# Performance work log

Measured on AMD Instinct MI355X. Metric: run time of the kernel, lower is better.

Reference implementation:

```python
import jax, jax.numpy as jnp
import numpy as np

BN_EPS = 1e-3
EPS = 1e-8
IGNORE = -1


def _head(x, w1, b1, g, be, w2, b2):
    # Linear -> BatchNorm1d (training: batch stats, biased var) -> ReLU -> Linear
    h = x @ w1 + b1
    mu = h.mean(axis=0)
    var = h.var(axis=0)  # biased, matches torch BN normalization
    h = (h - mu) * jax.lax.rsqrt(var + BN_EPS) * g + be
    h = jax.nn.relu(h)
    return h @ w2 + b2


def _bias_losses(a, b, mask):
    # faithful to compute_loss(bias_gt, bias_pred, mask); l1 and cosine are symmetric
    dist = jnp.sum(jnp.abs(a - b), axis=-1)
    denom = jnp.sum(mask) + EPS
    l1 = jnp.sum(dist * mask) / denom
    an = a / (jnp.linalg.norm(a, axis=-1, keepdims=True) + EPS)
    bn = b / (jnp.linalg.norm(b, axis=-1, keepdims=True) + EPS)
    cos = -jnp.sum(an * bn, axis=-1)
    cl = jnp.sum(cos * mask) / denom
    return l1, cl


def setup_inputs() -> dict:
    key = jax.random.key(0)
    ks = jax.random.split(key, 12)
    N, C, S = 1048576, 64, 20
    inp = {
        'feat': jax.random.normal(ks[0], (N, C), jnp.float32),
        'coord': jax.random.normal(ks[1], (N, 3), jnp.float32) * 2.0,
        'segment': jax.random.randint(ks[2], (N,), -1, S).astype(jnp.int32),
        'instance': jax.random.randint(ks[3], (N,), -1, 200).astype(jnp.int32),
        'instance_centroid': jax.random.normal(ks[4], (N, 3), jnp.float32) * 2.0,
        'w1_xy': jax.random.normal(ks[5], (C, C), jnp.float32) * 0.05,
        'b1_xy': jnp.zeros((C,), jnp.float32),
        'g_xy': jnp.ones((C,), jnp.float32),
        'be_xy': jnp.zeros((C,), jnp.float32),
        'w2_xy': jax.random.normal(ks[6], (C, 2), jnp.float32) * 0.05,
        'b2_xy': jnp.zeros((2,), jnp.float32),
        'w1_z': jax.random.normal(ks[7], (C, C), jnp.float32) * 0.05,
        'b1_z': jnp.zeros((C,), jnp.float32),
        'g_z': jnp.ones((C,), jnp.float32),
        'be_z': jnp.zeros((C,), jnp.float32),
        'w2_z': jax.random.normal(ks[8], (C, 1), jnp.float32) * 0.05,
        'b2_z': jnp.zeros((1,), jnp.float32),
        'w_seg': jax.random.normal(ks[9], (C, S), jnp.float32) * 0.05,
        'b_seg': jnp.zeros((S,), jnp.float32),
    }
    return inp


def reference(feat, coord, segment, instance, instance_centroid,
              w1_xy, b1_xy, g_xy, be_xy, w2_xy, b2_xy,
              w1_z, b1_z, g_z, be_z, w2_z, b2_z,
              w_seg, b_seg):
    bias_pred_xy = _head(feat, w1_xy, b1_xy, g_xy, be_xy, w2_xy, b2_xy)  # [N,2]
    bias_pred_z = _head(feat, w1_z, b1_z, g_z, be_z, w2_z, b2_z)         # [N,1]
    logit_pred = feat @ w_seg + b_seg                                     # [N,S]

    # cross-entropy with ignore_index=-1, unit class weights
    valid = (segment != IGNORE)
    tgt = jnp.where(valid, segment, 0)
    logp = jax.nn.log_softmax(logit_pred, axis=-1)
    nll = -jnp.take_along_axis(logp, tgt[:, None], axis=1)[:, 0]
    vf = valid.astype(logit_pred.dtype)
    seg_loss = jnp.sum(nll * vf) / jnp.sum(vf)

    mask = (instance != IGNORE).astype(feat.dtype)
    bias_gt = instance_centroid - coord
    l1_xy, cos_xy = _bias_losses(bias_gt[:, :2], bias_pred_xy, mask)
    l1_z, cos_z = _bias_losses(bias_gt[:, 2:3], bias_pred_z, mask)

    # faithful to original (bias_xy_l1 counted twice, xy cosine unused in total)
    loss = seg_loss + l1_xy + l1_xy + 0.5 * (l1_z + cos_z)
    return (loss, seg_loss, l1_xy, cos_xy, l1_z, cos_z)
```

## Files before the change

kernel.cpp:

```cpp
#include <hip/hip_runtime.h>
#include <hip/hip_bf16.h>

#define OFF_COLSUM 0
#define OFF_S      64
#define OFF_SHX    4160
#define OFF_SHZ    4224
#define OFF_ACC    4288
#define OFF_W1XS   4304
#define OFF_W1ZS   6352
#define OFF_WSEGS  8400

typedef __attribute__((ext_vector_type(8))) short bf16x8;
typedef __attribute__((ext_vector_type(4))) float f32x4;

__device__ __forceinline__ unsigned short f2bfh(float x) {
    __hip_bfloat16 h = __float2bfloat16(x);
    return *reinterpret_cast<unsigned short*>(&h);
}

union BF8 { bf16x8 v; unsigned short u[8]; };

__device__ __forceinline__ void gload_lds16(const void* g, void* l) {
    __builtin_amdgcn_global_load_lds((const __attribute__((address_space(1))) void*)g,
                                     (__attribute__((address_space(3))) void*)l, 16, 0, 0);
}


__global__ __launch_bounds__(256, 2) void k_stats(const float* __restrict__ feat,
                                                  int N, int ntiles, int tpb,
                                                  float* __restrict__ ws) {
    __shared__ __align__(16) float ftile[2][4096];
    const int t = threadIdx.x;
    const int lane = t & 63, l15 = lane & 15, grp = lane >> 4, wv = t >> 6;

    const f32x4 z4 = {0.f, 0.f, 0.f, 0.f};
    f32x4 acc[4] = {z4, z4, z4, z4};
    float csum = 0.f;

    const int l3 = l15 & 3;
    const int cb_base = l15 >> 2;
    const int g1x8 = (grp & 1) * 8;

    const int ti0 = blockIdx.x * tpb;
    const int tiend = min(ti0 + tpb, ntiles);

    auto stage = [&](int bufi, int ti) {
        const int row0 = ti * 64;
        if (row0 + 64 <= N) {
#pragma unroll
            for (int c = 0; c < 4; c++) {
                const int r = (wv * 4 + c) * 4 + grp;
                const int u = l15 ^ (r & 15);
                gload_lds16(&feat[(size_t)(row0 + r) * 64 + u * 4],
                            &ftile[bufi][(wv * 4 + c) * 256]);
            }
        } else {
#pragma unroll
            for (int u2 = 0; u2 < 4; u2++) {
                const int i = t + u2 * 256;
                const int r = i >> 4, u = (i & 15) ^ (r & 15);
                float4 v = make_float4(0.f, 0.f, 0.f, 0.f);
                if (row0 + r < N) v = *(const float4*)&feat[(size_t)(row0 + r) * 64 + u * 4];
                *(float4*)&ftile[bufi][i * 4] = v;
            }
        }
    };

    if (ti0 < tiend) stage(0, ti0);
    int cur = 0;
    for (int ti = ti0; ti < tiend; ++ti) {
        __syncthreads();
        if (ti + 1 < tiend) stage(cur ^ 1, ti + 1);
        const float* fb = ftile[cur];

        bf16x8 fr[4][2];
#pragma unroll
        for (int s = 0; s < 4; s++) {
            const int g = (wv + s) & 3;
            const int cb = (g * 4 + cb_base) ^ g1x8;
#pragma unroll
            for (int h = 0; h < 2; h++) {
                const int pbase = h * 32 + grp * 8;
                float vs[8];
#pragma unroll
                for (int kk = 0; kk < 8; kk++)
                    vs[kk] = fb[(pbase + kk) * 64 + ((cb ^ kk) << 2) + l3];
                BF8 fv;
#pragma unroll
                for (int kk = 0; kk < 8; kk++) fv.u[kk] = f2bfh(vs[kk]);
                fr[s][h] = fv.v;
                if (s == 0) {
#pragma unroll
                    for (int kk = 0; kk < 8; kk++) csum += vs[kk];
                }
            }
        }
#pragma unroll
        for (int s = 0; s < 4; s++) {
            acc[s] = __builtin_amdgcn_mfma_f32_16x16x32_bf16(fr[0][0], fr[s][0], acc[s], 0, 0, 0);
            acc[s] = __builtin_amdgcn_mfma_f32_16x16x32_bf16(fr[0][1], fr[s][1], acc[s], 0, 0, 0);
        }
        cur ^= 1;
    }

    float* S = ws + OFF_S;
#pragma unroll
    for (int s = 0; s < 4; s++) {
        const int gj = (wv + s) & 3;
#pragma unroll
        for (int r = 0; r < 4; r++)
            atomicAdd(&S[(wv * 16 + grp * 4 + r) * 64 + gj * 16 + l15], acc[s][r]);
    }
    csum += __shfl_xor(csum, 16);
    csum += __shfl_xor(csum, 32);
    if (grp == 0) atomicAdd(&ws[OFF_COLSUM + wv * 16 + l15], csum);
}

__global__ __launch_bounds__(256) void k_prep(
    const float* __restrict__ w1xy, const float* __restrict__ b1xy,
    const float* __restrict__ gxy,  const float* __restrict__ bexy,
    const float* __restrict__ w1z,  const float* __restrict__ b1z,
    const float* __restrict__ gz,   const float* __restrict__ bez,
    const float* __restrict__ wseg, float Nf, float* __restrict__ ws) {
    __shared__ float S[64][64];
    __shared__ float cs[64];
    const int t = threadIdx.x;

    for (int i = t; i < 4096; i += 256) ((float*)S)[i] = ws[OFF_S + i];
    if (t < 64) cs[t] = ws[OFF_COLSUM + t];
    __syncthreads();

    if (t < 128) {
        const int head = t >> 6, j = t & 63;
        const float* w1 = head ? w1z : w1xy;
        float w[64];
#pragma unroll
        for (int k = 0; k < 64; k++) w[k] = w1[k * 64 + j];
        float d = 0.f;
#pragma unroll
        for (int k = 0; k < 64; k++) d = fmaf(cs[k], w[k], d);
        float quad = 0.f;
#pragma unroll
        for (int k = 0; k < 64; k++) {
            float rd = 0.f;
#pragma unroll
            for (int l = 0; l < 64; l++) rd = fmaf(S[k][l], w[l], rd);
            quad = fmaf(w[k], rd, quad);
        }
        const float b1 = head ? b1z[j] : b1xy[j];
        const float mu  = d / Nf + b1;
        const float eh2 = quad / Nf + 2.f * b1 * d / Nf + b1 * b1;
        const float var = eh2 - mu * mu;
        const float g  = head ? gz[j]  : gxy[j];
        const float be = head ? bez[j] : bexy[j];
        const float sc = g * rsqrtf(var + 1e-3f);
        const float sh = be - mu * sc;
        ws[(head ? OFF_SHZ : OFF_SHX) + j] = sh;
        unsigned short* dst = (unsigned short*)(ws + (head ? OFF_W1ZS : OFF_W1XS));
#pragma unroll
        for (int k = 0; k < 64; k++) dst[j * 64 + k] = f2bfh(w[k] * sc);
    } else if (t < 160) {
        const int j = t - 128;
        unsigned short* dst = (unsigned short*)(ws + OFF_WSEGS);
        for (int k = 0; k < 64; k++)
            dst[j * 64 + k] = (j < 20) ? f2bfh(wseg[k * 20 + j]) : (unsigned short)0;
    }
}

__global__ __launch_bounds__(256, 2) void k_loss(
    const float* __restrict__ feat, const float* __restrict__ coord,
    const int* __restrict__ seg, const int* __restrict__ inst,
    const float* __restrict__ cent,
    const unsigned short* __restrict__ w1xs, const unsigned short* __restrict__ w1zs,
    const unsigned short* __restrict__ wsegs,
    const float* __restrict__ shxv, const float* __restrict__ shzv,
    const float* __restrict__ w2xy, const float* __restrict__ b2xy,
    const float* __restrict__ w2z,  const float* __restrict__ b2z,
    const float* __restrict__ bseg,
    int N, int ntiles, int tpb, float* __restrict__ acc) {
    __shared__ __align__(16) float ftile[2][4096];
    __shared__ float red[4][8];

    const int t = threadIdx.x;
    const int lane = t & 63, l15 = lane & 15, grp = lane >> 4, wv = t >> 6;

    bf16x8 ax[4][2], az[4][2], ag[2][2];
#pragma unroll
    for (int nt = 0; nt < 4; nt++)
#pragma unroll
        for (int h = 0; h < 2; h++) {
            ax[nt][h] = *(const bf16x8*)&w1xs[(nt * 16 + l15) * 64 + grp * 8 + h * 32];
            az[nt][h] = *(const bf16x8*)&w1zs[(nt * 16 + l15) * 64 + grp * 8 + h * 32];
        }
#pragma unroll
    for (int nt = 0; nt < 2; nt++)
#pragma unroll
        for (int h = 0; h < 2; h++)
            ag[nt][h] = *(const bf16x8*)&wsegs[(nt * 16 + l15) * 64 + grp * 8 + h * 32];

    float shx_c[4][4], shz_c[4][4], w20[4][4], w21[4][4], w2zc[4][4], bs_c[2][4];
#pragma unroll
    for (int nt = 0; nt < 4; nt++)
#pragma unroll
        for (int r = 0; r < 4; r++) {
            const int c = nt * 16 + grp * 4 + r;
            shx_c[nt][r] = shxv[c]; shz_c[nt][r] = shzv[c];
            w20[nt][r] = w2xy[c * 2]; w21[nt][r] = w2xy[c * 2 + 1];
            w2zc[nt][r] = w2z[c];
        }
#pragma unroll
    for (int nt = 0; nt < 2; nt++)
#pragma unroll
        for (int r = 0; r < 4; r++) {
            const int c = nt * 16 + grp * 4 + r;
            bs_c[nt][r] = (c < 20) ? bseg[c] : -1e30f;
        }
    const float pb0 = b2xy[0], pb1 = b2xy[1], pbz = b2z[0];

    float s_nll = 0.f, s_vf = 0.f, s_l1xy = 0.f, s_cosxy = 0.f;
    float s_l1z = 0.f, s_cosz = 0.f, s_mask = 0.f;

    const int ti0 = blockIdx.x * tpb;
    const int tiend = min(ti0 + tpb, ntiles);

    auto stage = [&](int bufi, int ti) {
        const int row0 = ti * 64;
        if (row0 + 64 <= N) {
#pragma unroll
            for (int c = 0; c < 4; c++) {
                const int r = (wv * 4 + c) * 4 + grp;
                const int u = l15 ^ (r & 15);
                gload_lds16(&feat[(size_t)(row0 + r) * 64 + u * 4],
                            &ftile[bufi][(wv * 4 + c) * 256]);
            }
        } else {
#pragma unroll
            for (int u2 = 0; u2 < 4; u2++) {
                const int i = t + u2 * 256;
                const int r = i >> 4, u = (i & 15) ^ (r & 15);
                float4 v = make_float4(0.f, 0.f, 0.f, 0.f);
                if (row0 + r < N) v = *(const float4*)&feat[(size_t)(row0 + r) * 64 + u * 4];
                *(float4*)&ftile[bufi][i * 4] = v;
            }
        }
    };

    int p_tg = -1, p_iv = -1;
    float p_c0 = 0.f, p_c1 = 0.f, p_c2 = 0.f, p_e0 = 0.f, p_e1 = 0.f, p_e2 = 0.f;
    auto ptload = [&](int ti) {
        const int gp = ti * 64 + wv * 16 + l15;
        const bool inb = (gp < N);
        p_tg = inb ? seg[gp] : -1;
        p_iv = inb ? inst[gp] : -1;
        if (inb) {
            p_c0 = coord[(size_t)gp * 3]; p_c1 = coord[(size_t)gp * 3 + 1]; p_c2 = coord[(size_t)gp * 3 + 2];
            p_e0 = cent[(size_t)gp * 3];  p_e1 = cent[(size_t)gp * 3 + 1];  p_e2 = cent[(size_t)gp * 3 + 2];
        } else {
            p_c0 = p_c1 = p_c2 = p_e0 = p_e1 = p_e2 = 0.f;
        }
    };

    if (ti0 < tiend) { stage(0, ti0); ptload(ti0); }
    int cur = 0;
    for (int ti = ti0; ti < tiend; ++ti) {
        const int tg = p_tg, iv = p_iv;
        const float c0 = p_c0, c1 = p_c1, c2 = p_c2, e0 = p_e0, e1 = p_e1, e2 = p_e2;

        __syncthreads();
        if (ti + 1 < tiend) { stage(cur ^ 1, ti + 1); ptload(ti + 1); }

        const int p = wv * 16 + l15;
        const float* fb = ftile[cur];
        const float4 q0 = *(const float4*)&fb[(p * 16 + ((grp * 2)     ^ l15)) * 4];
        const float4 q1 = *(const float4*)&fb[(p * 16 + ((grp * 2 + 1) ^ l15)) * 4];
        const float4 q2 = *(const float4*)&fb[(p * 16 + ((8 + grp * 2) ^ l15)) * 4];
        const float4 q3 = *(const float4*)&fb[(p * 16 + ((9 + grp * 2) ^ l15)) * 4];
        BF8 b0, b1;
        b0.u[0] = f2bfh(q0.x); b0.u[1] = f2bfh(q0.y); b0.u[2] = f2bfh(q0.z); b0.u[3] = f2bfh(q0.w);
        b0.u[4] = f2bfh(q1.x); b0.u[5] = f2bfh(q1.y); b0.u[6] = f2bfh(q1.z); b0.u[7] = f2bfh(q1.w);
        b1.u[0] = f2bfh(q2.x); b1.u[1] = f2bfh(q2.y); b1.u[2] = f2bfh(q2.z); b1.u[3] = f2bfh(q2.w);
        b1.u[4] = f2bfh(q3.x); b1.u[5] = f2bfh(q3.y); b1.u[6] = f2bfh(q3.z); b1.u[7] = f2bfh(q3.w);

        f32x4 cg0 = {bs_c[0][0], bs_c[0][1], bs_c[0][2], bs_c[0][3]};
        cg0 = __builtin_amdgcn_mfma_f32_16x16x32_bf16(ag[0][0], b0.v, cg0, 0, 0, 0);
        cg0 = __builtin_amdgcn_mfma_f32_16x16x32_bf16(ag[0][1], b1.v, cg0, 0, 0, 0);
        f32x4 cg1 = {bs_c[1][0], bs_c[1][1], bs_c[1][2], bs_c[1][3]};
        cg1 = __builtin_amdgcn_mfma_f32_16x16x32_bf16(ag[1][0], b0.v, cg1, 0, 0, 0);
        cg1 = __builtin_amdgcn_mfma_f32_16x16x32_bf16(ag[1][1], b1.v, cg1, 0, 0, 0);
        float lmax = cg0[0];
#pragma unroll
        for (int r = 1; r < 4; r++) lmax = fmaxf(lmax, cg0[r]);
#pragma unroll
        for (int r = 0; r < 4; r++) lmax = fmaxf(lmax, cg1[r]);
        lmax = fmaxf(lmax, __shfl_xor(lmax, 16));
        lmax = fmaxf(lmax, __shfl_xor(lmax, 32));
        float se = 0.f;
#pragma unroll
        for (int r = 0; r < 4; r++) se += __expf(cg0[r] - lmax);
#pragma unroll
        for (int r = 0; r < 4; r++) se += __expf(cg1[r] - lmax);
        se += __shfl_xor(se, 16); se += __shfl_xor(se, 32);
        const float lse = lmax + __logf(se);
        float lt = 0.f;
#pragma unroll
        for (int r = 0; r < 4; r++) lt += (grp * 4 + r == tg) ? cg0[r] : 0.f;
#pragma unroll
        for (int r = 0; r < 4; r++) lt += (16 + grp * 4 + r == tg) ? cg1[r] : 0.f;
        lt += __shfl_xor(lt, 16); lt += __shfl_xor(lt, 32);
        const float vf = (tg >= 0) ? 1.f : 0.f;
        s_nll += (lse - lt) * vf;
        s_vf += vf;

        float s0 = 0.f, s1 = 0.f, szv = 0.f;
#pragma unroll
        for (int nt = 0; nt < 4; nt++) {
            f32x4 cc = {shx_c[nt][0], shx_c[nt][1], shx_c[nt][2], shx_c[nt][3]};
            cc = __builtin_amdgcn_mfma_f32_16x16x32_bf16(ax[nt][0], b0.v, cc, 0, 0, 0);
            cc = __builtin_amdgcn_mfma_f32_16x16x32_bf16(ax[nt][1], b1.v, cc, 0, 0, 0);
#pragma unroll
            for (int r = 0; r < 4; r++) {
                const float hx = fmaxf(cc[r], 0.f);
                s0 = fmaf(hx, w20[nt][r], s0);
                s1 = fmaf(hx, w21[nt][r], s1);
            }
            f32x4 cz = {shz_c[nt][0], shz_c[nt][1], shz_c[nt][2], shz_c[nt][3]};
            cz = __builtin_amdgcn_mfma_f32_16x16x32_bf16(az[nt][0], b0.v, cz, 0, 0, 0);
            cz = __builtin_amdgcn_mfma_f32_16x16x32_bf16(az[nt][1], b1.v, cz, 0, 0, 0);
#pragma unroll
            for (int r = 0; r < 4; r++) {
                const float hz = fmaxf(cz[r], 0.f);
                szv = fmaf(hz, w2zc[nt][r], szv);
            }
        }
        s0 += __shfl_xor(s0, 16);  s0 += __shfl_xor(s0, 32);
        s1 += __shfl_xor(s1, 16);  s1 += __shfl_xor(s1, 32);
        szv += __shfl_xor(szv, 16); szv += __shfl_xor(szv, 32);
        const float p0 = s0 + pb0, p1 = s1 + pb1, pz = szv + pbz;

        const float mk = (iv >= 0) ? 1.f : 0.f;
        const float a0 = e0 - c0, a1 = e1 - c1, a2 = e2 - c2;
        s_l1xy += (fabsf(a0 - p0) + fabsf(a1 - p1)) * mk;
        const float na = sqrtf(a0 * a0 + a1 * a1) + 1e-8f;
        const float nb = sqrtf(p0 * p0 + p1 * p1) + 1e-8f;
        s_cosxy -= ((a0 * p0 + a1 * p1) / (na * nb)) * mk;
        s_l1z += fabsf(a2 - pz) * mk;
        const float naz = fabsf(a2) + 1e-8f, nbz = fabsf(pz) + 1e-8f;
        s_cosz -= ((a2 * pz) / (naz * nbz)) * mk;
        s_mask += mk;

        cur ^= 1;
    }

    float v[7] = {s_nll * 0.25f, s_vf * 0.25f, s_l1xy * 0.25f, s_cosxy * 0.25f,
                  s_l1z * 0.25f, s_cosz * 0.25f, s_mask * 0.25f};
#pragma unroll
    for (int i = 0; i < 7; i++) {
#pragma unroll
        for (int o = 32; o > 0; o >>= 1) v[i] += __shfl_down(v[i], o);
    }
    if (lane == 0) {
#pragma unroll
        for (int i = 0; i < 7; i++) red[wv][i] = v[i];
    }
    __syncthreads();
    if (t < 7) {
        float s = red[0][t] + red[1][t] + red[2][t] + red[3][t];
        atomicAdd(&acc[t], s);
    }
}

__global__ void k_fin(const float* __restrict__ acc, float* __restrict__ out) {
    const float sn = acc[0], sv = acc[1], sl1 = acc[2], scx = acc[3];
    const float slz = acc[4], scz_ = acc[5], sm = acc[6];
    const float segl = sn / sv;
    const float den = sm + 1e-8f;
    const float l1xy = sl1 / den, cosxy = scx / den;
    const float l1z = slz / den, cosz = scz_ / den;
    out[0] = segl + l1xy + l1xy + 0.5f * (l1z + cosz);
    out[1] = segl;
    out[2] = l1xy;
    out[3] = cosxy;
    out[4] = l1z;
    out[5] = cosz;
}

extern "C" void kernel_launch(void* const* d_in, const int* in_sizes, int n_in,
                              void* d_out, int out_size, void* d_ws, size_t ws_size,
                              hipStream_t stream) {
    const float* feat  = (const float*)d_in[0];
    const float* coord = (const float*)d_in[1];
    const int*   segm  = (const int*)d_in[2];
    const int*   inst  = (const int*)d_in[3];
    const float* cent  = (const float*)d_in[4];
    const float* w1xy  = (const float*)d_in[5];
    const float* b1xy  = (const float*)d_in[6];
    const float* gxy   = (const float*)d_in[7];
    const float* bexy  = (const float*)d_in[8];
    const float* w2xy  = (const float*)d_in[9];
    const float* b2xy  = (const float*)d_in[10];
    const float* w1z   = (const float*)d_in[11];
    const float* b1z   = (const float*)d_in[12];
    const float* gz    = (const float*)d_in[13];
    const float* bez   = (const float*)d_in[14];
    const float* w2z   = (const float*)d_in[15];
    const float* b2z   = (const float*)d_in[16];
    const float* wseg  = (const float*)d_in[17];
    const float* bseg  = (const float*)d_in[18];

    const int N = in_sizes[0] / 64;
    float* ws = (float*)d_ws;
    const int ntiles = (N + 63) >> 6;
    const int grid = 512;
    const int tpb = (ntiles + grid - 1) / grid;

    hipMemsetAsync(d_ws, 0, (OFF_S + 4096) * sizeof(float), stream);
    hipMemsetAsync((char*)d_ws + OFF_ACC * sizeof(float), 0, 8 * sizeof(float), stream);

    k_stats<<<grid, 256, 0, stream>>>(feat, N, ntiles, tpb, ws);
    k_prep<<<1, 256, 0, stream>>>(w1xy, b1xy, gxy, bexy, w1z, b1z, gz, bez, wseg,
                                  (float)N, ws);
    k_loss<<<grid, 256, 0, stream>>>(
        feat, coord, segm, inst, cent,
        (const unsigned short*)(ws + OFF_W1XS),
        (const unsigned short*)(ws + OFF_W1ZS),
        (const unsigned short*)(ws + OFF_WSEGS),
        ws + OFF_SHX, ws + OFF_SHZ,
        w2xy, b2xy, w2z, b2z, bseg, N, ntiles, tpb, ws + OFF_ACC);
    k_fin<<<1, 1, 0, stream>>>(ws + OFF_ACC, (float*)d_out);
}
```

Baseline: 176.3 us.

## Fold finalize into loss kernel via last-block counter, merge memsets, widen stats grid

Removes the separate single-thread finalize kernel by having the last block of the loss kernel, detected with an atomic done-counter, compute the final losses. The two workspace memsets become one contiguous memset by moving the accumulators next to the stats region. The stats kernel now runs 1024 blocks with a launch bound of 4 blocks per CU instead of 512 with 2. This saves one launch and one memset but adds a fence and atomic per block, and the higher occupancy bound may cause register spilling.

```diff
diff --git a/kernel.cpp b/kernel.cpp
--- a/kernel.cpp
+++ b/kernel.cpp
@@ -3,9 +3,11 @@
 
 #define OFF_COLSUM 0
 #define OFF_S      64
-#define OFF_SHX    4160
-#define OFF_SHZ    4224
-#define OFF_ACC    4288
+#define OFF_ACC    4160
+#define OFF_DONE   4168
+#define OFF_ZEND   4169
+#define OFF_SHX    4176
+#define OFF_SHZ    4240
 #define OFF_W1XS   4304
 #define OFF_W1ZS   6352
 #define OFF_WSEGS  8400
@@ -26,7 +28,7 @@
 }
 
 
-__global__ __launch_bounds__(256, 2) void k_stats(const float* __restrict__ feat,
+__global__ __launch_bounds__(256, 4) void k_stats(const float* __restrict__ feat,
                                                   int N, int ntiles, int tpb,
                                                   float* __restrict__ ws) {
     __shared__ __align__(16) float ftile[2][4096];
@@ -177,7 +179,7 @@
     const float* __restrict__ w2xy, const float* __restrict__ b2xy,
     const float* __restrict__ w2z,  const float* __restrict__ b2z,
     const float* __restrict__ bseg,
-    int N, int ntiles, int tpb, float* __restrict__ acc) {
+    int N, int ntiles, int tpb, float* __restrict__ acc, float* __restrict__ out) {
     __shared__ __align__(16) float ftile[2][4096];
     __shared__ float red[4][8];
 
@@ -367,21 +369,27 @@
         float s = red[0][t] + red[1][t] + red[2][t] + red[3][t];
         atomicAdd(&acc[t], s);
     }
-}
-
-__global__ void k_fin(const float* __restrict__ acc, float* __restrict__ out) {
-    const float sn = acc[0], sv = acc[1], sl1 = acc[2], scx = acc[3];
-    const float slz = acc[4], scz_ = acc[5], sm = acc[6];
-    const float segl = sn / sv;
-    const float den = sm + 1e-8f;
-    const float l1xy = sl1 / den, cosxy = scx / den;
-    const float l1z = slz / den, cosz = scz_ / den;
-    out[0] = segl + l1xy + l1xy + 0.5f * (l1z + cosz);
-    out[1] = segl;
-    out[2] = l1xy;
-    out[3] = cosxy;
-    out[4] = l1z;
-    out[5] = cosz;
+    __syncthreads();
+    if (t == 0) {
+        __threadfence();
+        int* done = (int*)(acc + (OFF_DONE - OFF_ACC));
+        if (atomicAdd(done, 1) == (int)gridDim.x - 1) {
+            __threadfence();
+            float sv[7];
+#pragma unroll
+            for (int i = 0; i < 7; i++) sv[i] = atomicAdd(&acc[i], 0.f);
+            const float segl = sv[0] / sv[1];
+            const float den = sv[6] + 1e-8f;
+            const float l1xy = sv[2] / den, cosxy = sv[3] / den;
+            const float l1z = sv[4] / den, cosz = sv[5] / den;
+            out[0] = segl + l1xy + l1xy + 0.5f * (l1z + cosz);
+            out[1] = segl;
+            out[2] = l1xy;
+            out[3] = cosxy;
+            out[4] = l1z;
+            out[5] = cosz;
+        }
+    }
 }
 
 extern "C" void kernel_launch(void* const* d_in, const int* in_sizes, int n_in,
@@ -410,21 +418,23 @@
     const int N = in_sizes[0] / 64;
     float* ws = (float*)d_ws;
     const int ntiles = (N + 63) >> 6;
-    const int grid = 512;
-    const int tpb = (ntiles + grid - 1) / grid;
-
-    hipMemsetAsync(d_ws, 0, (OFF_S + 4096) * sizeof(float), stream);
-    hipMemsetAsync((char*)d_ws + OFF_ACC * sizeof(float), 0, 8 * sizeof(float), stream);
-
-    k_stats<<<grid, 256, 0, stream>>>(feat, N, ntiles, tpb, ws);
+
+    const int grid_s = 1024;
+    const int tpb_s = (ntiles + grid_s - 1) / grid_s;
+    const int grid_l = 512;
+    const int tpb_l = (ntiles + grid_l - 1) / grid_l;
+
+    hipMemsetAsync(d_ws, 0, OFF_ZEND * sizeof(float), stream);
+
+    k_stats<<<grid_s, 256, 0, stream>>>(feat, N, ntiles, tpb_s, ws);
     k_prep<<<1, 256, 0, stream>>>(w1xy, b1xy, gxy, bexy, w1z, b1z, gz, bez, wseg,
                                   (float)N, ws);
-    k_loss<<<grid, 256, 0, stream>>>(
+    k_loss<<<grid_l, 256, 0, stream>>>(
         feat, coord, segm, inst, cent,
         (const unsigned short*)(ws + OFF_W1XS),
         (const unsigned short*)(ws + OFF_W1ZS),
         (const unsigned short*)(ws + OFF_WSEGS),
         ws + OFF_SHX, ws + OFF_SHZ,
-        w2xy, b2xy, w2z, b2z, bseg, N, ntiles, tpb, ws + OFF_ACC);
-    k_fin<<<1, 1, 0, stream>>>(ws + OFF_ACC, (float*)d_out);
-}
+        w2xy, b2xy, w2z, b2z, bseg, N, ntiles, tpb_l,
+        ws + OFF_ACC, (float*)d_out);
+}
```

After: 195.8 us. +11.0%, slower.
